# Kernel tuning notes

Measured on AMD Instinct MI355X. Metric: run time of the kernel, lower is better.

Reference implementation:

```python
import jax, jax.numpy as jnp
import numpy as np

E = 2          # e_layers
DM = 64        # d_model == emb_dim (hardcoded 64 in out_layer)
H = 8          # n_heads
DH = DM // H
DFF = 256      # d_ff
P = 16         # patch_size
STRIDE = P // 2
SL = 4096      # seq_len
NPATCH = (SL - P) // STRIDE + 1   # 511
PRED = 96
B, M = 8, 8
FACTOR = 5
EPS = 1e-5


def setup_inputs() -> dict:
    key = jax.random.key(0)
    ks = jax.random.split(key, 32)
    s = jnp.float32(0.02)
    f = lambda i, shape: jax.random.normal(ks[i], shape, jnp.float32)
    d = {
        "x_enc": f(0, (B, SL, M)),
        "x_mark_enc": f(1, (B, SL, 4)),
        "x_dec": f(2, (B, PRED, M)),
        "x_mark_dec": f(3, (B, PRED, 4)),
        # patch embedding  Linear(patch_size -> emb_dim)
        "in_W": f(4, (DM, P)) * s,
        "in_b": jnp.zeros((DM,), jnp.float32),
        # per-layer attention projections (stacked over e_layers)
        "Wq": f(5, (E, DM, DM)) * s, "bq": jnp.zeros((E, DM), jnp.float32),
        "Wk": f(6, (E, DM, DM)) * s, "bk": jnp.zeros((E, DM), jnp.float32),
        "Wv": f(7, (E, DM, DM)) * s, "bv": jnp.zeros((E, DM), jnp.float32),
        "Wo": f(8, (E, DM, DM)) * s, "bo": jnp.zeros((E, DM), jnp.float32),
        # FFN (Conv1d kernel=1 == Linear)
        "c1_W": f(9, (E, DFF, DM)) * s, "c1_b": jnp.zeros((E, DFF), jnp.float32),
        "c2_W": f(10, (E, DM, DFF)) * s, "c2_b": jnp.zeros((E, DM), jnp.float32),
        # layer norms
        "ln1_g": jnp.ones((E, DM), jnp.float32), "ln1_b": jnp.zeros((E, DM), jnp.float32),
        "ln2_g": jnp.ones((E, DM), jnp.float32), "ln2_b": jnp.zeros((E, DM), jnp.float32),
        "lnf_g": jnp.ones((DM,), jnp.float32), "lnf_b": jnp.zeros((DM,), jnp.float32),
        # decode head  Linear(64*num_patches -> pred_len)
        "out_W": f(11, (PRED, DM * NPATCH)) * s,
        "out_b": jnp.zeros((PRED,), jnp.float32),
    }
    return d


def _ln(x, g, b):
    mu = x.mean(-1, keepdims=True)
    var = ((x - mu) ** 2).mean(-1, keepdims=True)
    return (x - mu) * jax.lax.rsqrt(var + EPS) * g + b


def _prob_attn(q, k, v, key):
    # q,k,v: [Bn, H, L, Dh]  (ProbSparse attention, mask_flag=False)
    Bn, h, Lq, Dh = q.shape
    Lk = k.shape[2]
    U_part = min(int(FACTOR * np.ceil(np.log(Lk))), Lk)   # sampled keys per query
    u = min(int(FACTOR * np.ceil(np.log(Lq))), Lq)        # top-u active queries
    idx = jax.random.randint(key, (Lq, U_part), 0, Lk)
    k_sample = k[:, :, idx, :]                             # [Bn,H,Lq,U,Dh]
    qk_sample = jnp.einsum('bhld,bhlud->bhlu', q, k_sample)
    # sparsity measure: max - sum/L_K (as in torch code)
    sparsity = qk_sample.max(-1) - qk_sample.sum(-1) / jnp.float32(Lk)
    _, top_idx = jax.lax.top_k(sparsity, u)                # [Bn,H,u]
    q_red = jnp.take_along_axis(q, top_idx[..., None], axis=2)  # [Bn,H,u,Dh]
    scale = jax.lax.rsqrt(jnp.float32(Dh))
    scores = jnp.einsum('bhud,bhkd->bhuk', q_red, k) * scale    # [Bn,H,u,Lk]
    attn = jax.nn.softmax(scores, axis=-1)
    # lazy context: mean of V for inactive queries, attn@V for active ones
    ctx = jnp.broadcast_to(v.mean(axis=2, keepdims=True), q.shape)
    upd = jnp.einsum('bhuk,bhkd->bhud', attn, v)
    bi = jnp.arange(Bn)[:, None, None]
    hi = jnp.arange(h)[None, :, None]
    ctx = ctx.at[bi, hi, top_idx].set(upd)
    return ctx.transpose(0, 2, 1, 3)  # [Bn,L,H,Dh]


def reference(x_enc, x_mark_enc, x_dec, x_mark_dec, in_W, in_b, Wq, bq, Wk, bk,
              Wv, bv, Wo, bo, c1_W, c1_b, c2_W, c2_b, ln1_g, ln1_b, ln2_g, ln2_b,
              lnf_g, lnf_b, out_W, out_b):
    Bb, L, Mm = x_enc.shape
    x = x_enc.transpose(0, 2, 1)  # b l m -> b m l
    pidx = jnp.arange(NPATCH)[:, None] * STRIDE + jnp.arange(P)[None, :]
    patches = x[:, :, pidx]                         # [B,M,N,P] (unfold)
    z = patches.reshape(Bb * Mm, NPATCH, P) @ in_W.T + in_b  # [BM,N,DM]
    akey = jax.random.key(1)
    for e in range(E):
        q = (z @ Wq[e].T + bq[e]).reshape(Bb * Mm, NPATCH, H, DH).transpose(0, 2, 1, 3)
        k = (z @ Wk[e].T + bk[e]).reshape(Bb * Mm, NPATCH, H, DH).transpose(0, 2, 1, 3)
        v = (z @ Wv[e].T + bv[e]).reshape(Bb * Mm, NPATCH, H, DH).transpose(0, 2, 1, 3)
        ctx = _prob_attn(q, k, v, jax.random.fold_in(akey, e))
        new_x = ctx.reshape(Bb * Mm, NPATCH, DM) @ Wo[e].T + bo[e]
        x1 = _ln(z + new_x, ln1_g[e], ln1_b[e])
        y = jax.nn.gelu(x1 @ c1_W[e].T + c1_b[e], approximate=False)
        y = y @ c2_W[e].T + c2_b[e]
        z = _ln(x1 + y, ln2_g[e], ln2_b[e])
    z = _ln(z, lnf_g, lnf_b)
    out = z.reshape(Bb * Mm, -1) @ out_W.T + out_b   # [BM, pred_len]
    out = out.reshape(Bb, Mm, PRED).transpose(0, 2, 1)  # (b m) l -> b l m
    return out[:, -PRED:, :]
```

## Files before the change

kernel.cpp:

```cpp
#include <hip/hip_runtime.h>
#include <hip/hip_bf16.h>
#include <stdint.h>
#include <math.h>

typedef __hip_bfloat16 bf16;
typedef __attribute__((ext_vector_type(8))) short short8;
typedef __attribute__((ext_vector_type(4))) short short4v;
typedef __attribute__((ext_vector_type(4))) float fx4;

#define NP 511
#define UPART 35
#define NTOK 32704
#define NBITS 17885
#define GENB 140
#define LN_EPS 1e-5f

__host__ __device__ __forceinline__ void tf2x32(uint32_t k0, uint32_t k1,
                                                uint32_t x0, uint32_t x1,
                                                uint32_t* o0, uint32_t* o1) {
  uint32_t ks2 = k0 ^ k1 ^ 0x1BD11BDAu;
  x0 += k0; x1 += k1;
#define TFR(r) { x0 += x1; x1 = (x1 << (r)) | (x1 >> (32 - (r))); x1 ^= x0; }
  TFR(13) TFR(15) TFR(26) TFR(6)   x0 += k1;  x1 += ks2 + 1u;
  TFR(17) TFR(29) TFR(16) TFR(24)  x0 += ks2; x1 += k0 + 2u;
  TFR(13) TFR(15) TFR(26) TFR(6)   x0 += k0;  x1 += k1 + 3u;
  TFR(17) TFR(29) TFR(16) TFR(24)  x0 += k1;  x1 += ks2 + 4u;
  TFR(13) TFR(15) TFR(26) TFR(6)   x0 += ks2; x1 += k0 + 5u;
#undef TFR
  *o0 = x0; *o1 = x1;
}

__device__ __forceinline__ float ldin(const void* p, int i, int f32) {
  if (f32) return ((const float*)p)[i];
  return __bfloat162float(((const bf16*)p)[i]);
}
__device__ __forceinline__ unsigned short f2bf(float v) {
  uint32_t u = __builtin_bit_cast(uint32_t, v);
  u += 0x7fffu + ((u >> 16) & 1u);
  return (unsigned short)(u >> 16);
}
__device__ __forceinline__ float bfb2f(uint32_t h) {
  uint32_t u = h << 16;
  return __builtin_bit_cast(float, u);
}
__device__ __forceinline__ float lo16(uint32_t w) { return bfb2f(w & 0xFFFFu); }
__device__ __forceinline__ float hi16(uint32_t w) { return bfb2f(w >> 16); }
__device__ __forceinline__ uint32_t pack2(float a, float b) {
  return (uint32_t)f2bf(a) | ((uint32_t)f2bf(b) << 16);
}
__device__ __forceinline__ int lanes_below(unsigned long long m) {
  return __builtin_amdgcn_mbcnt_hi((uint32_t)(m >> 32),
         __builtin_amdgcn_mbcnt_lo((uint32_t)m, 0));
}

__global__ void zero_out_kernel(bf16* __restrict__ out, int n) {
  int i = blockIdx.x * 256 + threadIdx.x;
  if (i < n) out[i] = __float2bfloat16(0.f);
}

__global__ __launch_bounds__(256) void genidx_embed_kernel(
    int* __restrict__ idxT,
    uint32_t ka0, uint32_t ka1, uint32_t kb0, uint32_t kb1,
    const uint32_t* __restrict__ lnfg, int* __restrict__ flag,
    const void* __restrict__ xe, const void* __restrict__ inW,
    const void* __restrict__ inb, float* __restrict__ z) {
  if (blockIdx.x < GENB) {
    if (blockIdx.x == 0 && threadIdx.x == 0)
      flag[0] = (lnfg[0] == 0x3F800000u) ? 1 : 0;
    int i = blockIdx.x * 256 + threadIdx.x;
    if (i >= 2 * NBITS) return;
    int e = i / NBITS;
    uint32_t j = (uint32_t)(i - e * NBITS);
    uint32_t k0 = e ? kb0 : ka0, k1 = e ? kb1 : ka1;
    uint32_t o0, o1;
    tf2x32(k0, k1, 0u, j, &o0, &o1);
    uint32_t bits = o1;
    uint32_t hi = bits >> 16, lo = bits & 0xFFFFu;
    uint32_t off = ((hi % 511u) * 32u + (lo % 511u)) % 511u;
    int l = (int)(j / UPART), u = (int)(j % UPART);
    idxT[e * NBITS + u * NP + l] = (int)off;
    return;
  }
  __shared__ float xs[136 * 8];
  int f = (lnfg[0] == 0x3F800000u) ? 1 : 0;
  int bid = blockIdx.x - GENB;
  int b = bid >> 5, nt = bid & 31;
  int n0 = nt * 16;
  for (int i = threadIdx.x; i < 1088; i += 256) {
    int row = i >> 3, m = i & 7;
    int g = n0 * 8 + row;
    xs[i] = (g < 4096) ? ldin(xe, (b * 4096 + g) * 8 + m, f) : 0.f;
  }
  int d = threadIdx.x & 63, mg = threadIdx.x >> 6;
  float wreg[16];
#pragma unroll
  for (int p = 0; p < 16; ++p) wreg[p] = ldin(inW, d * 16 + p, f);
  float bd = ldin(inb, d, f);
  __syncthreads();
  for (int nl = 0; nl < 16; ++nl) {
    int n = n0 + nl;
    if (n >= NP) break;
#pragma unroll
    for (int mm = 0; mm < 2; ++mm) {
      int m = mg * 2 + mm;
      float acc = bd;
#pragma unroll
      for (int p = 0; p < 16; ++p)
        acc = fmaf(xs[(nl * 8 + p) * 8 + m], wreg[p], acc);
      int t = (b * 8 + m) * NP + n;
      z[(size_t)t * 64 + d] = acc;
    }
  }
}

__global__ __launch_bounds__(256) void qkv_kernel(
    const float* __restrict__ z,
    const void* __restrict__ Wq, const void* __restrict__ bq,
    const void* __restrict__ Wk, const void* __restrict__ bk,
    const void* __restrict__ Wv, const void* __restrict__ bv,
    bf16* __restrict__ qb, bf16* __restrict__ kb, bf16* __restrict__ vb,
    const int* __restrict__ flg, int e) {
  __shared__ short xb[64 * 72];
  __shared__ short wL[192 * 72];
  __shared__ float bqs[192];
  int f = flg[0];
  int t0 = blockIdx.x * 64;
  int tid = threadIdx.x;
  {
    const float4* xg = (const float4*)(z + (size_t)t0 * 64);
#pragma unroll
    for (int r = 0; r < 4; ++r) {
      int i4 = r * 256 + tid;
      float4 v = xg[i4];
      int t = (i4 * 4) >> 6, d = (i4 * 4) & 63;
      short4v h;
      h.x = (short)f2bf(v.x); h.y = (short)f2bf(v.y);
      h.z = (short)f2bf(v.z); h.w = (short)f2bf(v.w);
      *(short4v*)&xb[t * 72 + d] = h;
    }
  }
  if (!f) {
    const uint4* Wg0 = (const uint4*)((const bf16*)Wq + e * 4096);
    const uint4* Wg1 = (const uint4*)((const bf16*)Wk + e * 4096);
    const uint4* Wg2 = (const uint4*)((const bf16*)Wv + e * 4096);
#pragma unroll
    for (int r = 0; r < 2; ++r) {
      int i = r * 256 + tid;
      int row = i >> 3, c8 = (i & 7) * 8;
      *(uint4*)&wL[row * 72 + c8] = Wg0[i];
      *(uint4*)&wL[(64 + row) * 72 + c8] = Wg1[i];
      *(uint4*)&wL[(128 + row) * 72 + c8] = Wg2[i];
    }
  } else {
#pragma unroll
    for (int r = 0; r < 16; ++r) {
      int i = r * 256 + tid;
      int row = i >> 6, c = i & 63;
      wL[row * 72 + c] = (short)f2bf(((const float*)Wq)[e * 4096 + i]);
      wL[(64 + row) * 72 + c] = (short)f2bf(((const float*)Wk)[e * 4096 + i]);
      wL[(128 + row) * 72 + c] = (short)f2bf(((const float*)Wv)[e * 4096 + i]);
    }
  }
  if (tid < 192) {
    int t3 = tid >> 6, j = tid & 63;
    bqs[tid] = (t3 == 0) ? ldin(bq, e * 64 + j, f)
             : (t3 == 1) ? ldin(bk, e * 64 + j, f)
                         : ldin(bv, e * 64 + j, f);
  }
  __syncthreads();
  int lane = tid & 63, w = tid >> 6;
  int m0 = w * 16, col = lane & 15, quad = lane >> 4;
  short8 a0 = *(const short8*)&xb[(m0 + col) * 72 + quad * 8];
  short8 a1 = *(const short8*)&xb[(m0 + col) * 72 + 32 + quad * 8];
#pragma unroll
  for (int nt = 0; nt < 12; ++nt) {
    fx4 acc = {0.f, 0.f, 0.f, 0.f};
    short8 b0 = *(const short8*)&wL[(nt * 16 + col) * 72 + quad * 8];
    short8 b1 = *(const short8*)&wL[(nt * 16 + col) * 72 + 32 + quad * 8];
    acc = __builtin_amdgcn_mfma_f32_16x16x32_bf16(a0, b0, acc, 0, 0, 0);
    acc = __builtin_amdgcn_mfma_f32_16x16x32_bf16(a1, b1, acc, 0, 0, 0);
    int c = nt * 16 + col;
    int t3 = c >> 6, hd = c & 63, h = hd >> 3, d2 = hd & 7;
    bf16* base = (t3 == 0) ? qb : (t3 == 1) ? kb : vb;
    float bia = bqs[c];
#pragma unroll
    for (int reg = 0; reg < 4; ++reg) {
      int tok = t0 + m0 + quad * 4 + reg;
      int bm = tok / NP, n = tok - bm * NP;
      base[((size_t)(bm * 8 + h) * NP + n) * 8 + d2] =
          __float2bfloat16(acc[reg] + bia);
    }
  }
}

__global__ __launch_bounds__(1024, 8) void attn_fused_kernel(
    const bf16* __restrict__ qg, const bf16* __restrict__ kg,
    const bf16* __restrict__ vg, const int* __restrict__ idxT,
    bf16* __restrict__ ctx) {
  __shared__ uint32_t kkp[NP * 5 + 5];
  __shared__ uint32_t kvp[NP * 5 + 5];
  __shared__ float spars[512];
  __shared__ float mxB_s[512], smB_s[512];
  __shared__ float redv[256];
  __shared__ int topi[UPART];
  __shared__ float vmean[8];
  __shared__ unsigned char selflag[NP + 1];
  int bh = blockIdx.x;
  int bm = bh >> 3, h = bh & 7;
  size_t hb = (size_t)bh * NP * 8;
  int tid = threadIdx.x;
  int lane = tid & 63, wv = tid >> 6;
  if (tid < 512) {
    if (tid < NP) {
      uint4 b = ((const uint4*)(kg + hb))[tid];
      uint32_t* dk = kkp + tid * 5;
      dk[0] = b.x; dk[1] = b.y; dk[2] = b.z; dk[3] = b.w;
    }
  } else {
    int n = tid - 512;
    if (n < NP) {
      uint4 c = ((const uint4*)(vg + hb))[n];
      uint32_t* dv = kvp + n * 5;
      dv[0] = c.x; dv[1] = c.y; dv[2] = c.z; dv[3] = c.w;
    }
  }
  __syncthreads();
  float mxA = -1e30f, smA = 0.f;
  if (tid < NP) {
    int l = tid;
    uint4 a = ((const uint4*)(qg + hb))[l];
    float ql[8];
    ql[0] = lo16(a.x); ql[1] = hi16(a.x);
    ql[2] = lo16(a.y); ql[3] = hi16(a.y);
    ql[4] = lo16(a.z); ql[5] = hi16(a.z);
    ql[6] = lo16(a.w); ql[7] = hi16(a.w);
#pragma unroll 6
    for (int u = 0; u < 18; ++u) {
      int j = idxT[u * NP + l];
      j = ((unsigned)j > 510u) ? 0 : j;
      const uint32_t* kr = kkp + j * 5;
      uint32_t w0 = kr[0], w1 = kr[1], w2 = kr[2], w3 = kr[3];
      float dt = 0.f;
      dt = fmaf(ql[0], lo16(w0), dt); dt = fmaf(ql[1], hi16(w0), dt);
      dt = fmaf(ql[2], lo16(w1), dt); dt = fmaf(ql[3], hi16(w1), dt);
      dt = fmaf(ql[4], lo16(w2), dt); dt = fmaf(ql[5], hi16(w2), dt);
      dt = fmaf(ql[6], lo16(w3), dt); dt = fmaf(ql[7], hi16(w3), dt);
      mxA = fmaxf(mxA, dt); smA += dt;
    }
  } else if (tid >= 512 && tid < 512 + NP) {
    int l = tid - 512;
    uint4 a = ((const uint4*)(qg + hb))[l];
    float ql[8];
    ql[0] = lo16(a.x); ql[1] = hi16(a.x);
    ql[2] = lo16(a.y); ql[3] = hi16(a.y);
    ql[4] = lo16(a.z); ql[5] = hi16(a.z);
    ql[6] = lo16(a.w); ql[7] = hi16(a.w);
    float mxB = -1e30f, smB = 0.f;
#pragma unroll 6
    for (int u = 18; u < 35; ++u) {
      int j = idxT[u * NP + l];
      j = ((unsigned)j > 510u) ? 0 : j;
      const uint32_t* kr = kkp + j * 5;
      uint32_t w0 = kr[0], w1 = kr[1], w2 = kr[2], w3 = kr[3];
      float dt = 0.f;
      dt = fmaf(ql[0], lo16(w0), dt); dt = fmaf(ql[1], hi16(w0), dt);
      dt = fmaf(ql[2], lo16(w1), dt); dt = fmaf(ql[3], hi16(w1), dt);
      dt = fmaf(ql[4], lo16(w2), dt); dt = fmaf(ql[5], hi16(w2), dt);
      dt = fmaf(ql[6], lo16(w3), dt); dt = fmaf(ql[7], hi16(w3), dt);
      mxB = fmaxf(mxB, dt); smB += dt;
    }
    mxB_s[l] = mxB; smB_s[l] = smB;
  }
  __syncthreads();
  if (tid < NP) {
    spars[tid] = fmaxf(mxA, mxB_s[tid]) - (smA + smB_s[tid]) * (1.0f / 511.0f);
  } else if (tid >= 512 && tid < 768) {
    int tt = tid - 512;
    int d = tt & 7, pt = tt >> 3;
    int c = d >> 1, odd = d & 1;
    float s = 0.f;
    for (int n = pt; n < NP; n += 32) {
      uint32_t w = kvp[n * 5 + c];
      s += odd ? hi16(w) : lo16(w);
    }
    redv[tt] = s;
  }
  __syncthreads();
  if (tid < 64) {
    uint32_t key[8];
#pragma unroll
    for (int jj = 0; jj < 8; ++jj) {
      int ll = lane + jj * 64;
      if (ll < NP) {
        uint32_t u = __builtin_bit_cast(uint32_t, spars[ll]);
        key[jj] = (u & 0x80000000u) ? ~u : (u | 0x80000000u);
      } else key[jj] = 0u;
    }
    uint32_t p = 0u;
    for (int b = 31; b >= 0; --b) {
      uint32_t t = p | (1u << b);
      int cnt = 0;
#pragma unroll
      for (int jj = 0; jj < 8; ++jj)
        cnt += __popcll(__ballot(key[jj] >= t));
      if (cnt >= UPART) p = t;
    }
    int c1 = 0;
#pragma unroll
    for (int jj = 0; jj < 8; ++jj)
      c1 += __popcll(__ballot(key[jj] > p));
    int need = UPART - c1;
    int base = 0, taken = 0;
#pragma unroll
    for (int jj = 0; jj < 8; ++jj) {
      int ll = lane + jj * 64;
      bool gt = key[jj] > p;
      bool eq = key[jj] == p;
      unsigned long long meq = __ballot(eq);
      int beq = lanes_below(meq);
      bool sel = gt || (eq && (taken + beq) < need);
      unsigned long long msel = __ballot(sel);
      int pos = base + lanes_below(msel);
      if (sel) topi[pos] = ll;
      if (ll < NP) selflag[ll] = sel ? 1 : 0;
      base += __popcll(msel);
      taken += __popcll(meq);
    }
  } else if (tid >= 64 && tid < 72) {
    int d = tid - 64;
    float s = 0.f;
#pragma unroll
    for (int pt = 0; pt < 32; ++pt) s += redv[pt * 8 + d];
    vmean[d] = s * (1.0f / 511.0f);
  }
  __syncthreads();
  size_t cb = (size_t)bm * (NP * 64) + h * 8;
  if (tid < NP && !selflag[tid]) {
    uint4 pv;
    pv.x = pack2(vmean[0], vmean[1]);
    pv.y = pack2(vmean[2], vmean[3]);
    pv.z = pack2(vmean[4], vmean[5]);
    pv.w = pack2(vmean[6], vmean[7]);
    *(uint4*)(ctx + cb + (size_t)tid * 64) = pv;
  }
  const float scale = 0.35355339059327373f;
  int l0 = topi[wv];
  int l1 = topi[wv + 16];
  bool has3 = (wv + 32) < UPART;
  int l2 = has3 ? topi[wv + 32] : l0;
  l0 = ((unsigned)l0 > 510u) ? 0 : l0;
  l1 = ((unsigned)l1 > 510u) ? 0 : l1;
  l2 = ((unsigned)l2 > 510u) ? 0 : l2;
  const uint4* q4p = (const uint4*)(qg + hb);
  uint4 qv0 = q4p[l0];
  uint4 qv1 = q4p[l1];
  uint4 qv2 = q4p[l2];

  auto process = [&](uint4 a, int lsel) {
    float qs[8];
    qs[0] = lo16(a.x); qs[1] = hi16(a.x);
    qs[2] = lo16(a.y); qs[3] = hi16(a.y);
    qs[4] = lo16(a.z); qs[5] = hi16(a.z);
    qs[6] = lo16(a.w); qs[7] = hi16(a.w);
    float sreg[8];
    float mx = -1e30f;
#pragma unroll
    for (int s = 0; s < 8; ++s) {
      int j = lane + s * 64;
      int jc = (j > 510) ? 0 : j;
      const uint32_t* kr = kkp + jc * 5;
      uint32_t w0 = kr[0], w1 = kr[1], w2 = kr[2], w3 = kr[3];
      float d0 = qs[0] * lo16(w0);
      d0 = fmaf(qs[1], hi16(w0), d0);
      d0 = fmaf(qs[2], lo16(w1), d0);
      d0 = fmaf(qs[3], hi16(w1), d0);
      float d1 = qs[4] * lo16(w2);
      d1 = fmaf(qs[5], hi16(w2), d1);
      d1 = fmaf(qs[6], lo16(w3), d1);
      d1 = fmaf(qs[7], hi16(w3), d1);
      float sc = (d0 + d1) * scale;
      sreg[s] = (j > 510) ? -1e30f : sc;
      mx = fmaxf(mx, sreg[s]);
    }
    for (int off = 32; off; off >>= 1) mx = fmaxf(mx, __shfl_xor(mx, off));
    float ssum = 0.f, acc[8];
#pragma unroll
    for (int d2 = 0; d2 < 8; ++d2) acc[d2] = 0.f;
#pragma unroll
    for (int s = 0; s < 8; ++s) {
      int j = lane + s * 64;
      int jc = (j > 510) ? 0 : j;
      float w = __expf(sreg[s] - mx);
      ssum += w;
      const uint32_t* vr = kvp + jc * 5;
      uint32_t x0 = vr[0], x1 = vr[1], x2 = vr[2], x3 = vr[3];
      acc[0] = fmaf(w, lo16(x0), acc[0]); acc[1] = fmaf(w, hi16(x0), acc[1]);
      acc[2] = fmaf(w, lo16(x1), acc[2]); acc[3] = fmaf(w, hi16(x1), acc[3]);
      acc[4] = fmaf(w, lo16(x2), acc[4]); acc[5] = fmaf(w, hi16(x2), acc[5]);
      acc[6] = fmaf(w, lo16(x3), acc[6]); acc[7] = fmaf(w, hi16(x3), acc[7]);
    }
    for (int off = 32; off; off >>= 1) {
      ssum += __shfl_xor(ssum, off);
#pragma unroll
      for (int d2 = 0; d2 < 8; ++d2) acc[d2] += __shfl_xor(acc[d2], off);
    }
    if (lane == 0) {
      float inv = 1.0f / ssum;
      uint4 pv;
      pv.x = pack2(acc[0] * inv, acc[1] * inv);
      pv.y = pack2(acc[2] * inv, acc[3] * inv);
      pv.z = pack2(acc[4] * inv, acc[5] * inv);
      pv.w = pack2(acc[6] * inv, acc[7] * inv);
      *(uint4*)(ctx + cb + (size_t)lsel * 64) = pv;
    }
  };
  process(qv0, l0);
  process(qv1, l1);
  if (has3) process(qv2, l2);
}

__global__ __launch_bounds__(256) void oproj_ffn_kernel(
    const float* __restrict__ z, const bf16* __restrict__ ctx,
    const void* __restrict__ Wo, const void* __restrict__ bo,
    const void* __restrict__ l1g, const void* __restrict__ l1b,
    const void* __restrict__ W1, const void* __restrict__ b1,
    const void* __restrict__ W2, const void* __restrict__ b2,
    const void* __restrict__ g, const void* __restrict__ bb,
    float* __restrict__ zo, bf16* __restrict__ zfT,
    const void* __restrict__ lfg, const void* __restrict__ lfb,
    const int* __restrict__ flg, int e, int last) {
  __shared__ __align__(16) char smem[73728];
  short* cbL = (short*)smem;
  short* woL = (short*)(smem + 9216);
  float* zf  = (float*)(smem + 18432);
  short* wA  = (short*)smem;
  short* rB  = (short*)(smem + 36864);
  float* b1s = (float*)(smem + 70656);
  float* b2s  = b1s + 256;
  float* gs   = b2s + 64;
  float* bbs  = gs + 64;
  float* g2s  = bbs + 64;
  float* bb2s = g2s + 64;
  float* bos  = bb2s + 64;
  float* g1s  = bos + 64;
  float* bb1s = g1s + 64;
  int f = flg[0];
  int t0 = blockIdx.x * 64;
  int tid = threadIdx.x;
  {
    const uint4* cg = (const uint4*)(ctx + (size_t)t0 * 64);
#pragma unroll
    for (int r = 0; r < 2; ++r) {
      int i = r * 256 + tid;
      uint4 v = cg[i];
      int row = i >> 3, c8 = (i & 7) * 8;
      *(uint4*)&cbL[row * 72 + c8] = v;
    }
    const float4* zg = (const float4*)(z + (size_t)t0 * 64);
#pragma unroll
    for (int r = 0; r < 4; ++r) {
      int i4 = r * 256 + tid;
      float4 v = zg[i4];
      int t = (i4 * 4) >> 6, d = (i4 * 4) & 63;
      *(float4*)&zf[t * 64 + d] = v;
    }
  }
  if (!f) {
    const uint4* Wg = (const uint4*)((const bf16*)Wo + e * 4096);
#pragma unroll
    for (int r = 0; r < 2; ++r) {
      int i = r * 256 + tid;
      int row = i >> 3, c8 = (i & 7) * 8;
      *(uint4*)&woL[row * 72 + c8] = Wg[i];
    }
  } else {
#pragma unroll
    for (int r = 0; r < 16; ++r) {
      int i = r * 256 + tid;
      int row = i >> 6, c = i & 63;
      woL[row * 72 + c] = (short)f2bf(((const float*)Wo)[e * 4096 + i]);
    }
  }
  b1s[tid] = ldin(b1, e * 256 + tid, f);
  if (tid < 64) {
    b2s[tid] = ldin(b2, e * 64 + tid, f);
    gs[tid] = ldin(g, e * 64 + tid, f);
    bbs[tid] = ldin(bb, e * 64 + tid, f);
    g2s[tid] = ldin(lfg, tid, f);
    bb2s[tid] = ldin(lfb, tid, f);
    bos[tid] = ldin(bo, e * 64 + tid, f);
    g1s[tid] = ldin(l1g, e * 64 + tid, f);
    bb1s[tid] = ldin(l1b, e * 64 + tid, f);
  }
  __syncthreads();
  int lane = tid & 63, w = tid >> 6;
  int m0 = w * 16, col = lane & 15, quad = lane >> 4;
  float x1v[4][4];
  {
    short8 a0 = *(const short8*)&cbL[(m0 + col) * 72 + quad * 8];
    short8 a1 = *(const short8*)&cbL[(m0 + col) * 72 + 32 + quad * 8];
    fx4 vacc[4];
#pragma unroll
    for (int nt = 0; nt < 4; ++nt) {
      fx4 acc = {0.f, 0.f, 0.f, 0.f};
      short8 b0 = *(const short8*)&woL[(nt * 16 + col) * 72 + quad * 8];
      short8 b1f = *(const short8*)&woL[(nt * 16 + col) * 72 + 32 + quad * 8];
      acc = __builtin_amdgcn_mfma_f32_16x16x32_bf16(a0, b0, acc, 0, 0, 0);
      acc = __builtin_amdgcn_mfma_f32_16x16x32_bf16(a1, b1f, acc, 0, 0, 0);
      vacc[nt] = acc;
    }
    float vals[4][4];
    float ps[4], sq[4];
#pragma unroll
    for (int reg = 0; reg < 4; ++reg) { ps[reg] = 0.f; sq[reg] = 0.f; }
#pragma unroll
    for (int nt = 0; nt < 4; ++nt) {
      int d = nt * 16 + col;
#pragma unroll
      for (int reg = 0; reg < 4; ++reg) {
        int tl = m0 + quad * 4 + reg;
        float v = vacc[nt][reg] + bos[d] + zf[tl * 64 + d];
        vals[nt][reg] = v;
        ps[reg] += v; sq[reg] += v * v;
      }
    }
#pragma unroll
    for (int off = 1; off < 16; off <<= 1) {
#pragma unroll
      for (int reg = 0; reg < 4; ++reg) {
        ps[reg] += __shfl_xor(ps[reg], off);
        sq[reg] += __shfl_xor(sq[reg], off);
      }
    }
#pragma unroll
    for (int reg = 0; reg < 4; ++reg) {
      float mu = ps[reg] * (1.0f / 64.0f);
      float var = sq[reg] * (1.0f / 64.0f) - mu * mu;
      float rs = rsqrtf(fmaxf(var, 0.f) + LN_EPS);
#pragma unroll
      for (int nt = 0; nt < 4; ++nt) {
        int d = nt * 16 + col;
        x1v[nt][reg] = (vals[nt][reg] - mu) * rs * g1s[d] + bb1s[d];
      }
    }
#pragma unroll
    for (int nt = 0; nt < 4; ++nt) {
#pragma unroll
      for (int reg = 0; reg < 4; ++reg) {
        int tl = m0 + quad * 4 + reg;
        rB[tl * 72 + nt * 16 + col] = (short)f2bf(x1v[nt][reg]);
      }
    }
  }
  __syncthreads();
  if (!f) {
    const uint4* W1g = (const uint4*)((const bf16*)W1 + e * 16384);
#pragma unroll
    for (int r = 0; r < 8; ++r) {
      int i = r * 256 + tid;
      uint4 v = W1g[i];
      int j = i >> 3, k = (i & 7) * 8;
      *(uint4*)&wA[j * 72 + k] = v;
    }
  } else {
    for (int r = 0; r < 64; ++r) {
      int i = r * 256 + tid;
      int j = i >> 6, k = i & 63;
      wA[j * 72 + k] = (short)f2bf(((const float*)W1)[e * 16384 + i]);
    }
  }
  short8 a0 = *(const short8*)&rB[(m0 + col) * 72 + quad * 8];
  short8 a1 = *(const short8*)&rB[(m0 + col) * 72 + 32 + quad * 8];
  __syncthreads();
#pragma unroll 4
  for (int nt = 0; nt < 16; ++nt) {
    fx4 acc = {0.f, 0.f, 0.f, 0.f};
    short8 bf0 = *(const short8*)&wA[(nt * 16 + col) * 72 + quad * 8];
    short8 bf1 = *(const short8*)&wA[(nt * 16 + col) * 72 + 32 + quad * 8];
    acc = __builtin_amdgcn_mfma_f32_16x16x32_bf16(a0, bf0, acc, 0, 0, 0);
    acc = __builtin_amdgcn_mfma_f32_16x16x32_bf16(a1, bf1, acc, 0, 0, 0);
    int j = nt * 16 + col;
    float bj = b1s[j];
#pragma unroll
    for (int reg = 0; reg < 4; ++reg) {
      float a = acc[reg] + bj;
      float ge = 0.5f * a * (1.0f + erff(a * 0.70710678118654752f));
      rB[(m0 + quad * 4 + reg) * 264 + j] = (short)f2bf(ge);
    }
  }
  __syncthreads();
  if (!f) {
    const uint4* W2g = (const uint4*)((const bf16*)W2 + e * 16384);
#pragma unroll
    for (int r = 0; r < 8; ++r) {
      int i = r * 256 + tid;
      uint4 v2 = W2g[i];
      int dd = i >> 5, c = (i & 31) * 8;
      *(uint4*)&wA[dd * 264 + c] = v2;
    }
  } else {
    for (int r = 0; r < 64; ++r) {
      int i = r * 256 + tid;
      int dd = i >> 8, c = i & 255;
      wA[dd * 264 + c] = (short)f2bf(((const float*)W2)[e * 16384 + i]);
    }
  }
  __syncthreads();
  short8 af[8];
#pragma unroll
  for (int kt = 0; kt < 8; ++kt)
    af[kt] = *(const short8*)&rB[(m0 + col) * 264 + kt * 32 + quad * 8];
  fx4 vacc[4];
#pragma unroll
  for (int nt = 0; nt < 4; ++nt) {
    fx4 acc = {0.f, 0.f, 0.f, 0.f};
#pragma unroll
    for (int kt = 0; kt < 8; ++kt) {
      short8 bfr = *(const short8*)&wA[(nt * 16 + col) * 264 + kt * 32 + quad * 8];
      acc = __builtin_amdgcn_mfma_f32_16x16x32_bf16(af[kt], bfr, acc, 0, 0, 0);
    }
    vacc[nt] = acc;
  }
  float vals[4][4];
  float ps[4], sq[4];
#pragma unroll
  for (int reg = 0; reg < 4; ++reg) { ps[reg] = 0.f; sq[reg] = 0.f; }
#pragma unroll
  for (int nt = 0; nt < 4; ++nt) {
    int d = nt * 16 + col;
#pragma unroll
    for (int reg = 0; reg < 4; ++reg) {
      float v = vacc[nt][reg] + b2s[d] + x1v[nt][reg];
      vals[nt][reg] = v;
      ps[reg] += v; sq[reg] += v * v;
    }
  }
#pragma unroll
  for (int off = 1; off < 16; off <<= 1) {
#pragma unroll
    for (int reg = 0; reg < 4; ++reg) {
      ps[reg] += __shfl_xor(ps[reg], off);
      sq[reg] += __shfl_xor(sq[reg], off);
    }
  }
  if (!last) {
#pragma unroll
    for (int reg = 0; reg < 4; ++reg) {
      float mu = ps[reg] * (1.0f / 64.0f);
      float var = sq[reg] * (1.0f / 64.0f) - mu * mu;
      float rs = rsqrtf(fmaxf(var, 0.f) + LN_EPS);
      int tl = m0 + quad * 4 + reg;
#pragma unroll
      for (int nt = 0; nt < 4; ++nt) {
        int d = nt * 16 + col;
        zo[(size_t)(t0 + tl) * 64 + d] = (vals[nt][reg] - mu) * rs * gs[d] + bbs[d];
      }
    }
  } else {
    float ps2[4], sq2[4];
#pragma unroll
    for (int reg = 0; reg < 4; ++reg) { ps2[reg] = 0.f; sq2[reg] = 0.f; }
    float v2s[4][4];
#pragma unroll
    for (int reg = 0; reg < 4; ++reg) {
      float mu = ps[reg] * (1.0f / 64.0f);
      float var = sq[reg] * (1.0f / 64.0f) - mu * mu;
      float rs = rsqrtf(fmaxf(var, 0.f) + LN_EPS);
#pragma unroll
      for (int nt = 0; nt < 4; ++nt) {
        int d = nt * 16 + col;
        float v2 = (vals[nt][reg] - mu) * rs * gs[d] + bbs[d];
        v2s[nt][reg] = v2;
        ps2[reg] += v2; sq2[reg] += v2 * v2;
      }
    }
#pragma unroll
    for (int off = 1; off < 16; off <<= 1) {
#pragma unroll
      for (int reg = 0; reg < 4; ++reg) {
        ps2[reg] += __shfl_xor(ps2[reg], off);
        sq2[reg] += __shfl_xor(sq2[reg], off);
      }
    }
#pragma unroll
    for (int reg = 0; reg < 4; ++reg) {
      float mu = ps2[reg] * (1.0f / 64.0f);
      float var = sq2[reg] * (1.0f / 64.0f) - mu * mu;
      float rs = rsqrtf(fmaxf(var, 0.f) + LN_EPS);
      int tok = t0 + m0 + quad * 4 + reg;
      int bm = tok / NP, n = tok - bm * NP;
#pragma unroll
      for (int nt = 0; nt < 4; ++nt) {
        int d = nt * 16 + col;
        zfT[(size_t)n * 4096 + bm * 64 + d] =
            __float2bfloat16((v2s[nt][reg] - mu) * rs * g2s[d] + bb2s[d]);
      }
    }
  }
}

__global__ __launch_bounds__(256) void head1_kernel(
    const bf16* __restrict__ zfT, const void* __restrict__ W,
    float* __restrict__ partial, const int* __restrict__ flg) {
  __shared__ short aL[64 * 72];
  __shared__ short bL[96 * 72];
  int f = flg[0];
  int n = blockIdx.x;
  int tid = threadIdx.x;
  {
    const uint4* Ag = (const uint4*)(zfT + (size_t)n * 4096);
#pragma unroll
    for (int r = 0; r < 2; ++r) {
      int i = r * 256 + tid;
      uint4 v = Ag[i];
      int row = i >> 3, c = (i & 7) * 8;
      *(uint4*)&aL[row * 72 + c] = v;
    }
  }
  if (!f) {
    const uint4* Wg = (const uint4*)W;
#pragma unroll
    for (int r = 0; r < 3; ++r) {
      int i = r * 256 + tid;
      int p = i >> 3, c8 = i & 7;
      uint4 v = Wg[(size_t)p * 4088 + n * 8 + c8];
      *(uint4*)&bL[p * 72 + c8 * 8] = v;
    }
  } else {
    for (int r = 0; r < 24; ++r) {
      int i = r * 256 + tid;
      int p = i >> 6, c = i & 63;
      bL[p * 72 + c] = (short)f2bf(((const float*)W)[(size_t)p * 32704 + n * 64 + c]);
    }
  }
  __syncthreads();
  int lane = tid & 63, w = tid >> 6;
  int m0 = w * 16, col = lane & 15, quad = lane >> 4;
  short8 a0 = *(const short8*)&aL[(m0 + col) * 72 + quad * 8];
  short8 a1 = *(const short8*)&aL[(m0 + col) * 72 + 32 + quad * 8];
  float* pb = partial + (size_t)n * 6144;
#pragma unroll
  for (int nt = 0; nt < 6; ++nt) {
    fx4 acc = {0.f, 0.f, 0.f, 0.f};
    short8 b0 = *(const short8*)&bL[(nt * 16 + col) * 72 + quad * 8];
    short8 b1 = *(const short8*)&bL[(nt * 16 + col) * 72 + 32 + quad * 8];
    acc = __builtin_amdgcn_mfma_f32_16x16x32_bf16(a0, b0, acc, 0, 0, 0);
    acc = __builtin_amdgcn_mfma_f32_16x16x32_bf16(a1, b1, acc, 0, 0, 0);
#pragma unroll
    for (int reg = 0; reg < 4; ++reg)
      pb[(m0 + quad * 4 + reg) * 96 + nt * 16 + col] = acc[reg];
  }
}

__global__ __launch_bounds__(256) void head2_kernel(
    const float* __restrict__ partial, const void* __restrict__ bias,
    void* __restrict__ out, const int* __restrict__ flg) {
  __shared__ float red[4][64];
  int f = flg[0];
  int lane = threadIdx.x & 63, w = threadIdx.x >> 6;
  int j = blockIdx.x * 64 + lane;
  float acc = 0.f;
  for (int n = w; n < NP; n += 4)
    acc += partial[(size_t)n * 6144 + j];
  red[w][lane] = acc;
  __syncthreads();
  if (w == 0) {
    float s = red[0][lane] + red[1][lane] + red[2][lane] + red[3][lane];
    int bm = j / 96, p = j - bm * 96;
    float val = s + ldin(bias, p, f);
    int b = bm >> 3, m = bm & 7;
    int o = (b * 96 + p) * 8 + m;
    if (f) ((float*)out)[o] = val;
    else   ((bf16*)out)[o] = __float2bfloat16(val);
  }
}

extern "C" void kernel_launch(void* const* d_in, const int* in_sizes, int n_in,
                              void* d_out, int out_size, void* d_ws, size_t ws_size,
                              hipStream_t stream) {
  const void* xe  = d_in[0];
  const void* inW = d_in[4];
  const void* inb = d_in[5];
  const void* Wq  = d_in[6];
  const void* bq  = d_in[7];
  const void* Wk  = d_in[8];
  const void* bk  = d_in[9];
  const void* Wv  = d_in[10];
  const void* bv  = d_in[11];
  const void* Wo  = d_in[12];
  const void* bo  = d_in[13];
  const void* c1W = d_in[14];
  const void* c1b = d_in[15];
  const void* c2W = d_in[16];
  const void* c2b = d_in[17];
  const void* l1g = d_in[18];
  const void* l1b = d_in[19];
  const void* l2g = d_in[20];
  const void* l2b = d_in[21];
  const void* lfg = d_in[22];
  const void* lfb = d_in[23];
  const void* oW  = d_in[24];
  const void* obv = d_in[25];

  const size_t NF = (size_t)NTOK * 64;
  const size_t REQ = (3 * NF + 2 * NBITS + 32) * sizeof(float);
  if (ws_size < REQ) {
    zero_out_kernel<<<(out_size + 255) / 256, 256, 0, stream>>>((bf16*)d_out, out_size);
    return;
  }

  float* z   = (float*)d_ws;
  bf16* ctxb = (bf16*)(z + NF);
  bf16* qb   = (bf16*)(z + NF + NF / 2);
  bf16* kb   = (bf16*)(z + 2 * NF);
  bf16* vb   = (bf16*)(z + 2 * NF + NF / 2);
  int* idxb  = (int*)(z + 3 * NF);
  int* flg   = idxb + 2 * NBITS;
  bf16* zfT  = ctxb;
  float* partial = z;

  uint32_t ke[2][2];
  for (int e = 0; e < 2; ++e)
    tf2x32(0u, 1u, 0u, (uint32_t)e, &ke[e][0], &ke[e][1]);

  genidx_embed_kernel<<<GENB + 256, 256, 0, stream>>>(idxb,
      ke[0][0], ke[0][1], ke[1][0], ke[1][1], (const uint32_t*)lfg, flg,
      xe, inW, inb, z);

  for (int e = 0; e < 2; ++e) {
    qkv_kernel<<<NTOK / 64, 256, 0, stream>>>(z, Wq, bq, Wk, bk, Wv, bv,
        qb, kb, vb, flg, e);
    attn_fused_kernel<<<512, 1024, 0, stream>>>(qb, kb, vb, idxb + e * NBITS,
        ctxb);
    oproj_ffn_kernel<<<NTOK / 64, 256, 0, stream>>>(z, ctxb, Wo, bo, l1g, l1b,
        c1W, c1b, c2W, c2b, l2g, l2b, z, zfT, lfg, lfb, flg, e, e == 1);
  }
  head1_kernel<<<NP, 256, 0, stream>>>(zfT, oW, partial, flg);
  head2_kernel<<<96, 256, 0, stream>>>(partial, obv, d_out, flg);
}
```

Before: 297.3 us.

## Fuse QKV projection into attention kernel, computing per-head Q/K/V in LDS

Removes the separate QKV projection kernel and computes each head's 24 Q/K/V output channels inside the attention block using MFMA over the token chunk, writing results directly to shared memory. This eliminates the global write and re-read of bf16 Q/K/V and one launch per layer. In exchange, each of the eight head blocks per sequence re-reads and re-converts the full fp32 z slice, and the attention block takes on extra LDS and serialized chunk loops.

```diff
diff --git a/kernel.cpp b/kernel.cpp
--- a/kernel.cpp
+++ b/kernel.cpp
@@ -113,127 +113,101 @@
   }
 }
 
-__global__ __launch_bounds__(256) void qkv_kernel(
+__global__ __launch_bounds__(1024, 8) void attn_fused_kernel(
     const float* __restrict__ z,
     const void* __restrict__ Wq, const void* __restrict__ bq,
     const void* __restrict__ Wk, const void* __restrict__ bk,
     const void* __restrict__ Wv, const void* __restrict__ bv,
-    bf16* __restrict__ qb, bf16* __restrict__ kb, bf16* __restrict__ vb,
+    const int* __restrict__ idxT, bf16* __restrict__ ctx,
     const int* __restrict__ flg, int e) {
-  __shared__ short xb[64 * 72];
-  __shared__ short wL[192 * 72];
-  __shared__ float bqs[192];
-  int f = flg[0];
-  int t0 = blockIdx.x * 64;
-  int tid = threadIdx.x;
-  {
-    const float4* xg = (const float4*)(z + (size_t)t0 * 64);
-#pragma unroll
-    for (int r = 0; r < 4; ++r) {
-      int i4 = r * 256 + tid;
-      float4 v = xg[i4];
-      int t = (i4 * 4) >> 6, d = (i4 * 4) & 63;
-      short4v h;
-      h.x = (short)f2bf(v.x); h.y = (short)f2bf(v.y);
-      h.z = (short)f2bf(v.z); h.w = (short)f2bf(v.w);
-      *(short4v*)&xb[t * 72 + d] = h;
-    }
-  }
-  if (!f) {
-    const uint4* Wg0 = (const uint4*)((const bf16*)Wq + e * 4096);
-    const uint4* Wg1 = (const uint4*)((const bf16*)Wk + e * 4096);
-    const uint4* Wg2 = (const uint4*)((const bf16*)Wv + e * 4096);
-#pragma unroll
-    for (int r = 0; r < 2; ++r) {
-      int i = r * 256 + tid;
-      int row = i >> 3, c8 = (i & 7) * 8;
-      *(uint4*)&wL[row * 72 + c8] = Wg0[i];
-      *(uint4*)&wL[(64 + row) * 72 + c8] = Wg1[i];
-      *(uint4*)&wL[(128 + row) * 72 + c8] = Wg2[i];
-    }
-  } else {
-#pragma unroll
-    for (int r = 0; r < 16; ++r) {
-      int i = r * 256 + tid;
-      int row = i >> 6, c = i & 63;
-      wL[row * 72 + c] = (short)f2bf(((const float*)Wq)[e * 4096 + i]);
-      wL[(64 + row) * 72 + c] = (short)f2bf(((const float*)Wk)[e * 4096 + i]);
-      wL[(128 + row) * 72 + c] = (short)f2bf(((const float*)Wv)[e * 4096 + i]);
-    }
-  }
-  if (tid < 192) {
-    int t3 = tid >> 6, j = tid & 63;
-    bqs[tid] = (t3 == 0) ? ldin(bq, e * 64 + j, f)
-             : (t3 == 1) ? ldin(bk, e * 64 + j, f)
-                         : ldin(bv, e * 64 + j, f);
-  }
-  __syncthreads();
-  int lane = tid & 63, w = tid >> 6;
-  int m0 = w * 16, col = lane & 15, quad = lane >> 4;
-  short8 a0 = *(const short8*)&xb[(m0 + col) * 72 + quad * 8];
-  short8 a1 = *(const short8*)&xb[(m0 + col) * 72 + 32 + quad * 8];
-#pragma unroll
-  for (int nt = 0; nt < 12; ++nt) {
-    fx4 acc = {0.f, 0.f, 0.f, 0.f};
-    short8 b0 = *(const short8*)&wL[(nt * 16 + col) * 72 + quad * 8];
-    short8 b1 = *(const short8*)&wL[(nt * 16 + col) * 72 + 32 + quad * 8];
-    acc = __builtin_amdgcn_mfma_f32_16x16x32_bf16(a0, b0, acc, 0, 0, 0);
-    acc = __builtin_amdgcn_mfma_f32_16x16x32_bf16(a1, b1, acc, 0, 0, 0);
-    int c = nt * 16 + col;
-    int t3 = c >> 6, hd = c & 63, h = hd >> 3, d2 = hd & 7;
-    bf16* base = (t3 == 0) ? qb : (t3 == 1) ? kb : vb;
-    float bia = bqs[c];
-#pragma unroll
-    for (int reg = 0; reg < 4; ++reg) {
-      int tok = t0 + m0 + quad * 4 + reg;
-      int bm = tok / NP, n = tok - bm * NP;
-      base[((size_t)(bm * 8 + h) * NP + n) * 8 + d2] =
-          __float2bfloat16(acc[reg] + bia);
-    }
-  }
-}
-
-__global__ __launch_bounds__(1024, 8) void attn_fused_kernel(
-    const bf16* __restrict__ qg, const bf16* __restrict__ kg,
-    const bf16* __restrict__ vg, const int* __restrict__ idxT,
-    bf16* __restrict__ ctx) {
   __shared__ uint32_t kkp[NP * 5 + 5];
   __shared__ uint32_t kvp[NP * 5 + 5];
+  __shared__ uint32_t qld[NP * 5 + 5];
+  __shared__ short zb[128 * 72];
+  __shared__ short wB[32 * 72];
+  __shared__ float bqs2[32];
   __shared__ float spars[512];
   __shared__ float mxB_s[512], smB_s[512];
   __shared__ float redv[256];
   __shared__ int topi[UPART];
   __shared__ float vmean[8];
   __shared__ unsigned char selflag[NP + 1];
+  int f = flg[0];
   int bh = blockIdx.x;
   int bm = bh >> 3, h = bh & 7;
-  size_t hb = (size_t)bh * NP * 8;
   int tid = threadIdx.x;
   int lane = tid & 63, wv = tid >> 6;
-  if (tid < 512) {
-    if (tid < NP) {
-      uint4 b = ((const uint4*)(kg + hb))[tid];
-      uint32_t* dk = kkp + tid * 5;
-      dk[0] = b.x; dk[1] = b.y; dk[2] = b.z; dk[3] = b.w;
-    }
-  } else {
-    int n = tid - 512;
-    if (n < NP) {
-      uint4 c = ((const uint4*)(vg + hb))[n];
-      uint32_t* dv = kvp + n * 5;
-      dv[0] = c.x; dv[1] = c.y; dv[2] = c.z; dv[3] = c.w;
+  int col = lane & 15, quad = lane >> 4;
+  if (tid < 96) {
+    int row24 = tid >> 2, part = tid & 3;
+    if (!f) {
+      const bf16* src =
+          (row24 < 8)  ? (const bf16*)Wq + e * 4096 + (h * 8 + row24) * 64
+        : (row24 < 16) ? (const bf16*)Wk + e * 4096 + (h * 8 + row24 - 8) * 64
+                       : (const bf16*)Wv + e * 4096 + (h * 8 + row24 - 16) * 64;
+      uint4 v = ((const uint4*)src)[part];
+      *(uint4*)&wB[row24 * 72 + part * 16] = v;
+    } else {
+      const float* src =
+          (row24 < 8)  ? (const float*)Wq + e * 4096 + (h * 8 + row24) * 64
+        : (row24 < 16) ? (const float*)Wk + e * 4096 + (h * 8 + row24 - 8) * 64
+                       : (const float*)Wv + e * 4096 + (h * 8 + row24 - 16) * 64;
+      for (int c = 0; c < 16; ++c)
+        wB[row24 * 72 + part * 16 + c] = (short)f2bf(src[part * 16 + c]);
+    }
+  } else if (tid >= 128 && tid < 152) {
+    int ch = tid - 128;
+    bqs2[ch] = (ch < 8)  ? ldin(bq, e * 64 + h * 8 + ch, f)
+             : (ch < 16) ? ldin(bk, e * 64 + h * 8 + ch - 8, f)
+                         : ldin(bv, e * 64 + h * 8 + ch - 16, f);
+  }
+  int bt = wv & 1, tr = wv >> 1;
+  const float* zbase = z + (size_t)bm * NP * 64;
+  for (int nc = 0; nc < 4; ++nc) {
+    if (nc) __syncthreads();
+#pragma unroll
+    for (int r = 0; r < 2; ++r) {
+      int i4 = r * 1024 + tid;
+      int lr = i4 >> 4, d4 = (i4 & 15) * 4;
+      int n = nc * 128 + lr;
+      float4 v;
+      if (n < NP) v = *(const float4*)(zbase + (size_t)n * 64 + d4);
+      else        v = make_float4(0.f, 0.f, 0.f, 0.f);
+      short4v hh;
+      hh.x = (short)f2bf(v.x); hh.y = (short)f2bf(v.y);
+      hh.z = (short)f2bf(v.z); hh.w = (short)f2bf(v.w);
+      *(short4v*)&zb[lr * 72 + d4] = hh;
+    }
+    __syncthreads();
+    short8 a0 = *(const short8*)&zb[(tr * 16 + col) * 72 + quad * 8];
+    short8 a1 = *(const short8*)&zb[(tr * 16 + col) * 72 + 32 + quad * 8];
+    short8 b0 = *(const short8*)&wB[(bt * 16 + col) * 72 + quad * 8];
+    short8 b1 = *(const short8*)&wB[(bt * 16 + col) * 72 + 32 + quad * 8];
+    fx4 acc = {0.f, 0.f, 0.f, 0.f};
+    acc = __builtin_amdgcn_mfma_f32_16x16x32_bf16(a0, b0, acc, 0, 0, 0);
+    acc = __builtin_amdgcn_mfma_f32_16x16x32_bf16(a1, b1, acc, 0, 0, 0);
+    int ch = bt * 16 + col;
+    if (ch < 24) {
+      float bia = bqs2[ch];
+      bf16* dst = (ch < 8) ? (bf16*)qld : (ch < 16) ? (bf16*)kkp : (bf16*)kvp;
+      int d2 = ch & 7;
+#pragma unroll
+      for (int reg = 0; reg < 4; ++reg) {
+        int n = nc * 128 + tr * 16 + quad * 4 + reg;
+        if (n < NP) dst[n * 10 + d2] = __float2bfloat16(acc[reg] + bia);
+      }
     }
   }
   __syncthreads();
   float mxA = -1e30f, smA = 0.f;
   if (tid < NP) {
     int l = tid;
-    uint4 a = ((const uint4*)(qg + hb))[l];
+    const uint32_t* qp = qld + l * 5;
     float ql[8];
-    ql[0] = lo16(a.x); ql[1] = hi16(a.x);
-    ql[2] = lo16(a.y); ql[3] = hi16(a.y);
-    ql[4] = lo16(a.z); ql[5] = hi16(a.z);
-    ql[6] = lo16(a.w); ql[7] = hi16(a.w);
+    ql[0] = lo16(qp[0]); ql[1] = hi16(qp[0]);
+    ql[2] = lo16(qp[1]); ql[3] = hi16(qp[1]);
+    ql[4] = lo16(qp[2]); ql[5] = hi16(qp[2]);
+    ql[6] = lo16(qp[3]); ql[7] = hi16(qp[3]);
 #pragma unroll 6
     for (int u = 0; u < 18; ++u) {
       int j = idxT[u * NP + l];
@@ -249,12 +223,12 @@
     }
   } else if (tid >= 512 && tid < 512 + NP) {
     int l = tid - 512;
-    uint4 a = ((const uint4*)(qg + hb))[l];
+    const uint32_t* qp = qld + l * 5;
     float ql[8];
-    ql[0] = lo16(a.x); ql[1] = hi16(a.x);
-    ql[2] = lo16(a.y); ql[3] = hi16(a.y);
-    ql[4] = lo16(a.z); ql[5] = hi16(a.z);
-    ql[6] = lo16(a.w); ql[7] = hi16(a.w);
+    ql[0] = lo16(qp[0]); ql[1] = hi16(qp[0]);
+    ql[2] = lo16(qp[1]); ql[3] = hi16(qp[1]);
+    ql[4] = lo16(qp[2]); ql[5] = hi16(qp[2]);
+    ql[6] = lo16(qp[3]); ql[7] = hi16(qp[3]);
     float mxB = -1e30f, smB = 0.f;
 #pragma unroll 6
     for (int u = 18; u < 35; ++u) {
@@ -351,10 +325,10 @@
   l0 = ((unsigned)l0 > 510u) ? 0 : l0;
   l1 = ((unsigned)l1 > 510u) ? 0 : l1;
   l2 = ((unsigned)l2 > 510u) ? 0 : l2;
-  const uint4* q4p = (const uint4*)(qg + hb);
-  uint4 qv0 = q4p[l0];
-  uint4 qv1 = q4p[l1];
-  uint4 qv2 = q4p[l2];
+  uint4 qv0, qv1, qv2;
+  { const uint32_t* p = qld + l0 * 5; qv0.x = p[0]; qv0.y = p[1]; qv0.z = p[2]; qv0.w = p[3]; }
+  { const uint32_t* p = qld + l1 * 5; qv1.x = p[0]; qv1.y = p[1]; qv1.z = p[2]; qv1.w = p[3]; }
+  { const uint32_t* p = qld + l2 * 5; qv2.x = p[0]; qv2.y = p[1]; qv2.z = p[2]; qv2.w = p[3]; }
 
   auto process = [&](uint4 a, int lsel) {
     float qs[8];
@@ -811,9 +785,6 @@
 
   float* z   = (float*)d_ws;
   bf16* ctxb = (bf16*)(z + NF);
-  bf16* qb   = (bf16*)(z + NF + NF / 2);
-  bf16* kb   = (bf16*)(z + 2 * NF);
-  bf16* vb   = (bf16*)(z + 2 * NF + NF / 2);
   int* idxb  = (int*)(z + 3 * NF);
   int* flg   = idxb + 2 * NBITS;
   bf16* zfT  = ctxb;
@@ -828,10 +799,8 @@
       xe, inW, inb, z);
 
   for (int e = 0; e < 2; ++e) {
-    qkv_kernel<<<NTOK / 64, 256, 0, stream>>>(z, Wq, bq, Wk, bk, Wv, bv,
-        qb, kb, vb, flg, e);
-    attn_fused_kernel<<<512, 1024, 0, stream>>>(qb, kb, vb, idxb + e * NBITS,
-        ctxb);
+    attn_fused_kernel<<<512, 1024, 0, stream>>>(z, Wq, bq, Wk, bk, Wv, bv,
+        idxb + e * NBITS, ctxb, flg, e);
     oproj_ffn_kernel<<<NTOK / 64, 256, 0, stream>>>(z, ctxb, Wo, bo, l1g, l1b,
         c1W, c1b, c2W, c2b, l2g, l2b, z, zfT, lfg, lfb, flg, e, e == 1);
   }
```

Measured after the change: 296.1 us. No clear change (-0.4%).
